# Kernel optimization log

Hardware: AMD Instinct MI355X
Metric: run time of the kernel (lower is better)

Reference implementation:

```python
import jax, jax.numpy as jnp
import numpy as np
from jax import lax

B, N, C = 8, 4096, 96
STRIDE, NSAMPLE, RADIUS = 4, 16, 0.1
C2 = 2 * C            # out_channels = 192 (also transfer in/out channels)
NPOINT = N // STRIDE  # 1024
EPS = 1e-5


def _fps(p, npoint):
    """Furthest point sampling. p: [B,N,3] -> idx [B,npoint] (starts at index 0)."""
    b, n, _ = p.shape
    def body(carry, _):
        mind, last = carry                       # [b,n], [b]
        lp = p[jnp.arange(b), last]              # [b,3]
        d = jnp.sum((p - lp[:, None, :]) ** 2, -1)
        mind = jnp.minimum(mind, d)
        nxt = jnp.argmax(mind, axis=1).astype(jnp.int32)
        return (mind, nxt), last
    init = (jnp.full((b, n), 1e10, p.dtype), jnp.zeros((b,), jnp.int32))
    (_, _), idxs = lax.scan(body, init, None, length=npoint)
    return jnp.transpose(idxs)                   # [b, npoint]


def _ball_query(new_p, p, radius, nsample):
    """First-nsample-in-index-order neighbors within radius; pad with first found."""
    n = p.shape[1]
    d2 = jnp.sum((new_p[:, :, None, :] - p[:, None, :, :]) ** 2, -1)  # [B,NP,N]
    order = jnp.where(d2 < radius * radius, jnp.arange(n, dtype=jnp.int32), n)
    vals, _ = lax.top_k(-order, nsample)         # k smallest 'order' values
    srt = -vals                                  # ascending valid indices, n = invalid
    return jnp.where(srt < n, srt, srt[..., :1]).astype(jnp.int32)


def _bn(y, g, b, m, v):
    """Eval-mode BatchNorm over channel axis 1."""
    shape = (1, -1) + (1,) * (y.ndim - 2)
    return (y - m.reshape(shape)) * (g.reshape(shape) / jnp.sqrt(v.reshape(shape) + EPS)) + b.reshape(shape)


def setup_inputs() -> dict:
    key = jax.random.key(0)
    ks = jax.random.split(key, 12)
    s = 1.0 / np.sqrt(C2)
    return {
        "p": jax.random.uniform(ks[0], (B, N, 3), jnp.float32),
        "x": jax.random.normal(ks[1], (B, C, N), jnp.float32),
        "Wt": jax.random.normal(ks[2], (C2, C2), jnp.float32) * s,
        "gt": 1.0 + 0.1 * jax.random.normal(ks[3], (C2,), jnp.float32),
        "bt": 0.1 * jax.random.normal(ks[4], (C2,), jnp.float32),
        "mt": 0.1 * jax.random.normal(ks[5], (C2,), jnp.float32),
        "vt": jax.random.uniform(ks[6], (C2,), jnp.float32, 0.5, 1.5),
        "Wc": jax.random.normal(ks[7], (C2, C2), jnp.float32) * s,
        "gc": 1.0 + 0.1 * jax.random.normal(ks[8], (C2,), jnp.float32),
        "bc": 0.1 * jax.random.normal(ks[9], (C2,), jnp.float32),
        "mc": 0.1 * jax.random.normal(ks[10], (C2,), jnp.float32),
        "vc": jax.random.uniform(ks[11], (C2,), jnp.float32, 0.5, 1.5),
    }


def reference(p, x, Wt, gt, bt, mt, vt, Wc, gc, bc, mc, vc):
    b = p.shape[0]
    bidx = jnp.arange(b)[:, None]
    # --- FPS sample + gather centers ---
    samp = _fps(p, NPOINT)                       # [B,NP]
    new_p = p[bidx, samp]                        # [B,NP,3]
    # --- ball-query grouping ---
    nbr = _ball_query(new_p, p, RADIUS, NSAMPLE)  # [B,NP,NS]
    bidx2 = jnp.arange(b)[:, None, None]
    gp = p[bidx2, nbr]                           # [B,NP,NS,3]
    dp = jnp.transpose(gp - new_p[:, :, None, :], (0, 3, 1, 2))  # [B,3,NP,NS]
    xt = jnp.transpose(x, (0, 2, 1))             # [B,N,C]
    gx = jnp.transpose(xt[bidx2, nbr], (0, 3, 1, 2))             # [B,C,NP,NS]
    cx = jnp.transpose(xt[bidx, samp], (0, 2, 1))[..., None]     # [B,C,NP,1]
    xj = jnp.concatenate([jnp.broadcast_to(cx, gx.shape), gx], axis=1)  # [B,2C,NP,NS]
    # --- act + transfer (1x1 conv + BN + relu) ---
    xj = jax.nn.relu(xj)
    xj = jax.nn.relu(_bn(jnp.einsum('oc,bcgs->bogs', Wt, xj), gt, bt, mt, vt))
    # --- PosPool sin/cos positional encoding ---
    fd = C2 // 6
    dim_mat = jnp.float32(500.0) ** (jnp.arange(fd, dtype=jnp.float32) / fd)
    pos = (50.0 * dp)[..., None] / dim_mat       # [B,3,NP,NS,fd]
    emb = jnp.concatenate([jnp.sin(pos), jnp.cos(pos)], -1)      # [B,3,NP,NS,2fd]
    emb = jnp.transpose(emb, (0, 1, 4, 2, 3)).reshape(xj.shape)  # [B,C2,NP,NS]
    agg = xj * emb + emb
    # --- max + mean pool over neighbors ---
    pooled = jnp.max(agg, -1) + jnp.mean(agg, -1)                # [B,C2,NP]
    # --- act + convs (1x1 conv + BN + relu) ---
    out = jax.nn.relu(_bn(jnp.einsum('oc,bcg->bog', Wc, jax.nn.relu(pooled)), gc, bc, mc, vc))
    return new_p, out
```

## Files before the change

### kernel.cpp

```cpp
#include <hip/hip_runtime.h>
#include <math.h>

#define BB 8
#define NN 4096
#define CC 96
#define C2 192
#define NP 1024
#define NS 16
#define FPT 8

#define SAMP_OFF   0u
#define NBR_OFF    32768u
#define WSW_OFF    655360u
#define B1_OFF     802816u
#define WCT_OFF    803584u
#define B2_OFF     951040u
#define ZT_OFF     958464u

template<int CTRL, int RM>
__device__ __forceinline__ unsigned long long dpp_mov64(unsigned long long k) {
    int tlo = __builtin_amdgcn_update_dpp(0, (int)(unsigned)(k & 0xffffffffull),
                                          CTRL, RM, 0xf, false);
    int thi = __builtin_amdgcn_update_dpp(0, (int)(unsigned)(k >> 32),
                                          CTRL, RM, 0xf, false);
    return ((unsigned long long)(unsigned)thi << 32) | (unsigned)tlo;
}

__global__ __launch_bounds__(512) void fps_prep_kernel(
        const float* __restrict__ p,
        const float* __restrict__ Wt, const float* __restrict__ gt,
        const float* __restrict__ bt, const float* __restrict__ mt,
        const float* __restrict__ vt, const float* __restrict__ Wc,
        const float* __restrict__ gc, const float* __restrict__ bc,
        const float* __restrict__ mc, const float* __restrict__ vc,
        float* __restrict__ Ws, float* __restrict__ beta1,
        float* __restrict__ WcT, float* __restrict__ beta2,
        int* __restrict__ samp, float* __restrict__ out) {
    if (blockIdx.x >= BB) {
        int i = (blockIdx.x - BB) * 512 + threadIdx.x;
        if (i < C2) {
            float s1 = gt[i] / sqrtf(vt[i] + 1e-5f);
            beta1[i] = bt[i] - mt[i] * s1;
            float s2 = gc[i] / sqrtf(vc[i] + 1e-5f);
            beta2[i] = bc[i] - mc[i] * s2;
        }
        if (i < 384 * 96) {
            int r = i / 96, c = i - r * 96;
            int o = (r < C2) ? r : r - C2;
            float s1 = gt[o] / sqrtf(vt[o] + 1e-5f);
            float w = (r < C2) ? Wt[o * C2 + c] : Wt[o * C2 + 96 + c];
            Ws[i] = w * s1;
        }
        if (i < C2 * C2) {
            int o = i / C2, c = i - o * C2;
            float s2 = gc[o] / sqrtf(vc[o] + 1e-5f);
            WcT[c * C2 + o] = Wc[i] * s2;
        }
        return;
    }
    int b = blockIdx.x;
    const float* pb = p + (size_t)b * NN * 3;
    __shared__ unsigned long long redk[2][8];
    __shared__ float4 redc[2][8];
    int tid = threadIdx.x;
    int jbase = tid * FPT;

    float c24[24];
    const float4* pb4 = (const float4*)(pb + (size_t)jbase * 3);
    #pragma unroll
    for (int i = 0; i < 6; ++i) ((float4*)c24)[i] = pb4[i];
    float px[FPT], py[FPT], pz[FPT], mind[FPT];
    #pragma unroll
    for (int i = 0; i < FPT; ++i) {
        px[i] = c24[3*i+0]; py[i] = c24[3*i+1]; pz[i] = c24[3*i+2];
        mind[i] = 1e10f;
    }

    int last = 0;
    float lx = pb[0], ly = pb[1], lz = pb[2];
    unsigned inv_base = 4095u - (unsigned)jbase;

    for (int it = 0; it < NP; ++it) {
        if (tid == 0) {
            samp[b * NP + it] = last;
            size_t o3 = ((size_t)b * NP + it) * 3;
            out[o3 + 0] = lx; out[o3 + 1] = ly; out[o3 + 2] = lz;
        }
        float m[FPT];
        #pragma unroll
        for (int i = 0; i < FPT; ++i) {
            float dx = __fsub_rn(px[i], lx);
            float dy = __fsub_rn(py[i], ly);
            float dz = __fsub_rn(pz[i], lz);
            float d = __fadd_rn(__fadd_rn(__fmul_rn(dx, dx), __fmul_rn(dy, dy)),
                                __fmul_rn(dz, dz));
            float mi = fminf(mind[i], d);
            mind[i] = mi;
            m[i] = mi;
        }
        float v4[4]; int i4v[4];
        #pragma unroll
        for (int q = 0; q < 4; ++q) {
            bool t = m[2*q+1] > m[2*q];
            v4[q] = t ? m[2*q+1] : m[2*q];
            i4v[q] = t ? 2*q+1 : 2*q;
        }
        float v2a[2]; int i2v[2];
        #pragma unroll
        for (int q = 0; q < 2; ++q) {
            bool t = v4[2*q+1] > v4[2*q];
            v2a[q] = t ? v4[2*q+1] : v4[2*q];
            i2v[q] = t ? i4v[2*q+1] : i4v[2*q];
        }
        bool tf = v2a[1] > v2a[0];
        float bv = tf ? v2a[1] : v2a[0];
        int ii  = tf ? i2v[1] : i2v[0];
        unsigned long long key =
            ((unsigned long long)__float_as_uint(bv) << 32)
            | (unsigned long long)(inv_base - (unsigned)ii);

        unsigned long long red = key, t;
        t = dpp_mov64<0x111, 0xf>(red); red = (t > red) ? t : red;
        t = dpp_mov64<0x112, 0xf>(red); red = (t > red) ? t : red;
        t = dpp_mov64<0x114, 0xf>(red); red = (t > red) ? t : red;
        t = dpp_mov64<0x118, 0xf>(red); red = (t > red) ? t : red;
        t = dpp_mov64<0x142, 0xa>(red); red = (t > red) ? t : red;
        t = dpp_mov64<0x143, 0xc>(red); red = (t > red) ? t : red;

        unsigned rlo = (unsigned)__builtin_amdgcn_readlane((int)(unsigned)(red & 0xffffffffull), 63);
        unsigned rhi = (unsigned)__builtin_amdgcn_readlane((int)(unsigned)(red >> 32), 63);
        unsigned long long wkey = ((unsigned long long)rhi << 32) | rlo;
        int buf = it & 1;
        if (key == wkey) {
            int wv = tid >> 6;
            redk[buf][wv] = wkey;
            redc[buf][wv] = make_float4(px[ii], py[ii], pz[ii], 0.0f);
        }
        __syncthreads();

        unsigned long long k0 = redk[buf][0], k1 = redk[buf][1];
        unsigned long long k2 = redk[buf][2], k3 = redk[buf][3];
        unsigned long long k4 = redk[buf][4], k5 = redk[buf][5];
        unsigned long long k6 = redk[buf][6], k7 = redk[buf][7];
        float4 c0 = redc[buf][0], c1 = redc[buf][1];
        float4 c2 = redc[buf][2], c3 = redc[buf][3];
        float4 c4 = redc[buf][4], c5 = redc[buf][5];
        float4 c6 = redc[buf][6], c7 = redc[buf][7];
        #define MRG(ka, ca, kb, cb) { bool tm = (kb) > (ka); \
            ka = tm ? (kb) : (ka); \
            ca.x = tm ? cb.x : ca.x; ca.y = tm ? cb.y : ca.y; ca.z = tm ? cb.z : ca.z; }
        MRG(k0, c0, k1, c1); MRG(k2, c2, k3, c3);
        MRG(k4, c4, k5, c5); MRG(k6, c6, k7, c7);
        MRG(k0, c0, k2, c2); MRG(k4, c4, k6, c6);
        MRG(k0, c0, k4, c4);
        #undef MRG
        last = 4095 - (int)(unsigned)(k0 & 0xffffffffull);
        lx = c0.x; ly = c0.y; lz = c0.z;
    }
}

__global__ __launch_bounds__(256) void bq_gemm_kernel(
        const float* __restrict__ p, const float* __restrict__ newp,
        int* __restrict__ nbr,
        const float* __restrict__ x, const float* __restrict__ Ws,
        float* __restrict__ zt) {
    __shared__ float smem[12352];
    int tid = threadIdx.x;

    if (blockIdx.x < 2048) {
        float* sx = smem;
        float* sy = smem + NN;
        float* sz = smem + 2 * NN;
        int blk = blockIdx.x;
        int b = blk >> 8;
        const float* pb = p + (size_t)b * NN * 3;
        for (int idx = tid; idx < NN; idx += 256) {
            sx[idx] = pb[idx * 3 + 0];
            sy[idx] = pb[idx * 3 + 1];
            sz[idx] = pb[idx * 3 + 2];
        }
        __syncthreads();
        int wave = tid >> 6, lane = tid & 63;
        int g = (blk & 255) * 4 + wave;
        int gidx = b * NP + g;
        float cx = newp[(size_t)gidx * 3 + 0];
        float cy = newp[(size_t)gidx * 3 + 1];
        float cz = newp[(size_t)gidx * 3 + 2];
        const float R2 = 0.01f;
        int cnt = 0, first = -1;
        for (int chunk = 0; chunk < NN / 64 && cnt < NS; ++chunk) {
            int j = chunk * 64 + lane;
            float dx = __fsub_rn(cx, sx[j]);
            float dy = __fsub_rn(cy, sy[j]);
            float dz = __fsub_rn(cz, sz[j]);
            float d2 = __fadd_rn(__fadd_rn(__fmul_rn(dx, dx), __fmul_rn(dy, dy)),
                                 __fmul_rn(dz, dz));
            unsigned long long mask = __ballot(d2 < R2);
            while (mask && cnt < NS) {
                int bit = __ffsll(mask) - 1;
                mask &= mask - 1;
                int idx = chunk * 64 + bit;
                if (first < 0) first = idx;
                if (lane == 0) nbr[(size_t)gidx * NS + cnt] = idx;
                ++cnt;
            }
        }
        if (lane == 0) {
            for (int i = cnt; i < NS; ++i) nbr[(size_t)gidx * NS + i] = first;
        }
    } else {
        float* xt = smem;
        float* wt = smem + 6144;
        int g = blockIdx.x - 2048;
        int b = g & 7;
        int t2 = g >> 3;
        int ob = t2 >> 6;
        int jt = t2 & 63;

        for (int idx = tid; idx < 96 * 64; idx += 256) {
            int c = idx >> 6, j = idx & 63;
            xt[c * 64 + j] = fmaxf(x[((size_t)b * CC + c) * NN + jt * 64 + j], 0.0f);
        }
        for (int idx = tid; idx < 64 * 96; idx += 256) {
            int r = idx / 96, c = idx - r * 96;
            wt[r * 97 + c] = Ws[(ob * 64 + r) * 96 + c];
        }
        __syncthreads();

        int ty = tid >> 4, tx = tid & 15;
        float acc[4][4] = {};
        for (int k = 0; k < 96; ++k) {
            float a0 = wt[(ty * 4 + 0) * 97 + k];
            float a1 = wt[(ty * 4 + 1) * 97 + k];
            float a2 = wt[(ty * 4 + 2) * 97 + k];
            float a3 = wt[(ty * 4 + 3) * 97 + k];
            float4 bv = *(const float4*)&xt[k * 64 + tx * 4];
            acc[0][0] = fmaf(a0, bv.x, acc[0][0]); acc[0][1] = fmaf(a0, bv.y, acc[0][1]);
            acc[0][2] = fmaf(a0, bv.z, acc[0][2]); acc[0][3] = fmaf(a0, bv.w, acc[0][3]);
            acc[1][0] = fmaf(a1, bv.x, acc[1][0]); acc[1][1] = fmaf(a1, bv.y, acc[1][1]);
            acc[1][2] = fmaf(a1, bv.z, acc[1][2]); acc[1][3] = fmaf(a1, bv.w, acc[1][3]);
            acc[2][0] = fmaf(a2, bv.x, acc[2][0]); acc[2][1] = fmaf(a2, bv.y, acc[2][1]);
            acc[2][2] = fmaf(a2, bv.z, acc[2][2]); acc[2][3] = fmaf(a2, bv.w, acc[2][3]);
            acc[3][0] = fmaf(a3, bv.x, acc[3][0]); acc[3][1] = fmaf(a3, bv.y, acc[3][1]);
            acc[3][2] = fmaf(a3, bv.z, acc[3][2]); acc[3][3] = fmaf(a3, bv.w, acc[3][3]);
        }
        for (int jj = 0; jj < 4; ++jj) {
            int j = jt * 64 + tx * 4 + jj;
            float4 v = make_float4(acc[0][jj], acc[1][jj], acc[2][jj], acc[3][jj]);
            *(float4*)&zt[((size_t)b * NN + j) * 384 + ob * 64 + ty * 4] = v;
        }
    }
}

__global__ __launch_bounds__(192) void fused_kernel(const float* __restrict__ p,
                                                    const float* __restrict__ newp,
                                                    const int* __restrict__ samp,
                                                    const int* __restrict__ nbr,
                                                    const float* __restrict__ zt,
                                                    const float* __restrict__ beta1,
                                                    const float* __restrict__ WcT,
                                                    const float* __restrict__ beta2,
                                                    float* __restrict__ out) {
    int blk = blockIdx.x;
    int b = blk >> 10, g = blk & 1023;
    int tid = threadIdx.x;
    __shared__ float dp[3][NS];
    __shared__ int nb[NS];
    __shared__ float pl[C2];

    if (tid < NS) {
        int j = nbr[(size_t)blk * NS + tid];
        nb[tid] = j;
        dp[0][tid] = p[((size_t)b * NN + j) * 3 + 0] - newp[(size_t)blk * 3 + 0];
        dp[1][tid] = p[((size_t)b * NN + j) * 3 + 1] - newp[(size_t)blk * 3 + 1];
        dp[2][tid] = p[((size_t)b * NN + j) * 3 + 2] - newp[(size_t)blk * 3 + 2];
    }
    __syncthreads();

    int o = tid;
    int sidx = samp[blk];
    float zc = zt[((size_t)b * NN + sidx) * 384 + o];
    float bet = beta1[o];
    int axis = o >> 6;
    int k = o & 63;
    int kk = (k < 32) ? k : k - 32;
    float dim = powf(500.0f, (float)kk * (1.0f / 32.0f));

    float mx = -3.4e38f, sm = 0.0f;
    for (int s = 0; s < NS; ++s) {
        float zn = zt[((size_t)b * NN + nb[s]) * 384 + C2 + o];
        float t = fmaxf(zc + zn + bet, 0.0f);
        float pos = (50.0f * dp[axis][s]) / dim;
        float e = (k < 32) ? sinf(pos) : cosf(pos);
        float a = fmaf(t, e, e);
        mx = fmaxf(mx, a);
        sm += a;
    }
    pl[o] = fmaxf(mx + sm * (1.0f / 16.0f), 0.0f);
    __syncthreads();

    float acc = 0.0f;
    for (int c = 0; c < C2; ++c) acc = fmaf(WcT[c * C2 + o], pl[c], acc);
    float res = fmaxf(acc + beta2[o], 0.0f);
    out[BB * NP * 3 + ((size_t)b * C2 + o) * NP + g] = res;
}

extern "C" void kernel_launch(void* const* d_in, const int* in_sizes, int n_in,
                              void* d_out, int out_size, void* d_ws, size_t ws_size,
                              hipStream_t stream) {
    (void)in_sizes; (void)n_in; (void)out_size; (void)ws_size;
    const float* p  = (const float*)d_in[0];
    const float* x  = (const float*)d_in[1];
    const float* Wt = (const float*)d_in[2];
    const float* gt = (const float*)d_in[3];
    const float* bt = (const float*)d_in[4];
    const float* mt = (const float*)d_in[5];
    const float* vt = (const float*)d_in[6];
    const float* Wc = (const float*)d_in[7];
    const float* gc = (const float*)d_in[8];
    const float* bc = (const float*)d_in[9];
    const float* mc = (const float*)d_in[10];
    const float* vc = (const float*)d_in[11];
    float* out = (float*)d_out;
    char* ws = (char*)d_ws;

    int*   samp  = (int*)(ws + SAMP_OFF);
    int*   nbr   = (int*)(ws + NBR_OFF);
    float* Ws    = (float*)(ws + WSW_OFF);
    float* beta1 = (float*)(ws + B1_OFF);
    float* WcT   = (float*)(ws + WCT_OFF);
    float* beta2 = (float*)(ws + B2_OFF);
    float* zt    = (float*)(ws + ZT_OFF);
    const float* newp = out;

    fps_prep_kernel<<<dim3(BB + 72), dim3(512), 0, stream>>>(
        p, Wt, gt, bt, mt, vt, Wc, gc, bc, mc, vc,
        Ws, beta1, WcT, beta2, samp, out);
    bq_gemm_kernel<<<dim3(2048 + 3072), dim3(256), 0, stream>>>(
        p, newp, nbr, x, Ws, zt);
    fused_kernel<<<dim3(BB * NP), dim3(192), 0, stream>>>(
        p, newp, samp, nbr, zt, beta1, WcT, beta2, out);
}
```

Baseline: 1.198 ms.

## Overlap GEMM with FPS in one launch and shrink FPS reduction to 4 waves

The transfer GEMM now runs in the same launch as furthest point sampling, so its blocks can fill the GPU while the 8 serial FPS blocks run. BN scaling of Wt is folded into the GEMM tile load, which removes the intermediate Ws buffer. FPS drops to 256 threads with 16 points each and replaces the 64-bit key DPP reduction with a float max reduction plus a ballot, which shortens the per-iteration critical path. Ball query becomes its own kernel after FPS. The risks are that GEMM blocks may contend with the FPS blocks for CU resources, and that per-thread register pressure in FPS rises.

```diff
diff --git a/kernel.cpp b/kernel.cpp
--- a/kernel.cpp
+++ b/kernel.cpp
@@ -7,7 +7,7 @@
 #define C2 192
 #define NP 1024
 #define NS 16
-#define FPT 8
+#define PPT 16
 
 #define SAMP_OFF   0u
 #define NBR_OFF    32768u
@@ -17,213 +17,52 @@
 #define B2_OFF     951040u
 #define ZT_OFF     958464u
 
+#define GEMM_OFF   152
+
 template<int CTRL, int RM>
-__device__ __forceinline__ unsigned long long dpp_mov64(unsigned long long k) {
-    int tlo = __builtin_amdgcn_update_dpp(0, (int)(unsigned)(k & 0xffffffffull),
-                                          CTRL, RM, 0xf, false);
-    int thi = __builtin_amdgcn_update_dpp(0, (int)(unsigned)(k >> 32),
-                                          CTRL, RM, 0xf, false);
-    return ((unsigned long long)(unsigned)thi << 32) | (unsigned)tlo;
-}
-
-__global__ __launch_bounds__(512) void fps_prep_kernel(
-        const float* __restrict__ p,
+__device__ __forceinline__ float dpp_maxf(float v) {
+    int t = __builtin_amdgcn_update_dpp(0, __float_as_int(v), CTRL, RM, 0xf, false);
+    return fmaxf(v, __int_as_float(t));
+}
+
+__global__ __launch_bounds__(256) void fps_prep_gemm_kernel(
+        const float* __restrict__ p, const float* __restrict__ x,
         const float* __restrict__ Wt, const float* __restrict__ gt,
         const float* __restrict__ bt, const float* __restrict__ mt,
         const float* __restrict__ vt, const float* __restrict__ Wc,
         const float* __restrict__ gc, const float* __restrict__ bc,
         const float* __restrict__ mc, const float* __restrict__ vc,
-        float* __restrict__ Ws, float* __restrict__ beta1,
-        float* __restrict__ WcT, float* __restrict__ beta2,
+        float* __restrict__ beta1, float* __restrict__ WcT,
+        float* __restrict__ beta2, float* __restrict__ zt,
         int* __restrict__ samp, float* __restrict__ out) {
-    if (blockIdx.x >= BB) {
-        int i = (blockIdx.x - BB) * 512 + threadIdx.x;
-        if (i < C2) {
-            float s1 = gt[i] / sqrtf(vt[i] + 1e-5f);
-            beta1[i] = bt[i] - mt[i] * s1;
-            float s2 = gc[i] / sqrtf(vc[i] + 1e-5f);
-            beta2[i] = bc[i] - mc[i] * s2;
-        }
-        if (i < 384 * 96) {
-            int r = i / 96, c = i - r * 96;
-            int o = (r < C2) ? r : r - C2;
-            float s1 = gt[o] / sqrtf(vt[o] + 1e-5f);
-            float w = (r < C2) ? Wt[o * C2 + c] : Wt[o * C2 + 96 + c];
-            Ws[i] = w * s1;
-        }
-        if (i < C2 * C2) {
-            int o = i / C2, c = i - o * C2;
-            float s2 = gc[o] / sqrtf(vc[o] + 1e-5f);
-            WcT[c * C2 + o] = Wc[i] * s2;
-        }
-        return;
-    }
-    int b = blockIdx.x;
-    const float* pb = p + (size_t)b * NN * 3;
-    __shared__ unsigned long long redk[2][8];
-    __shared__ float4 redc[2][8];
     int tid = threadIdx.x;
-    int jbase = tid * FPT;
-
-    float c24[24];
-    const float4* pb4 = (const float4*)(pb + (size_t)jbase * 3);
-    #pragma unroll
-    for (int i = 0; i < 6; ++i) ((float4*)c24)[i] = pb4[i];
-    float px[FPT], py[FPT], pz[FPT], mind[FPT];
-    #pragma unroll
-    for (int i = 0; i < FPT; ++i) {
-        px[i] = c24[3*i+0]; py[i] = c24[3*i+1]; pz[i] = c24[3*i+2];
-        mind[i] = 1e10f;
-    }
-
-    int last = 0;
-    float lx = pb[0], ly = pb[1], lz = pb[2];
-    unsigned inv_base = 4095u - (unsigned)jbase;
-
-    for (int it = 0; it < NP; ++it) {
-        if (tid == 0) {
-            samp[b * NP + it] = last;
-            size_t o3 = ((size_t)b * NP + it) * 3;
-            out[o3 + 0] = lx; out[o3 + 1] = ly; out[o3 + 2] = lz;
-        }
-        float m[FPT];
-        #pragma unroll
-        for (int i = 0; i < FPT; ++i) {
-            float dx = __fsub_rn(px[i], lx);
-            float dy = __fsub_rn(py[i], ly);
-            float dz = __fsub_rn(pz[i], lz);
-            float d = __fadd_rn(__fadd_rn(__fmul_rn(dx, dx), __fmul_rn(dy, dy)),
-                                __fmul_rn(dz, dz));
-            float mi = fminf(mind[i], d);
-            mind[i] = mi;
-            m[i] = mi;
-        }
-        float v4[4]; int i4v[4];
-        #pragma unroll
-        for (int q = 0; q < 4; ++q) {
-            bool t = m[2*q+1] > m[2*q];
-            v4[q] = t ? m[2*q+1] : m[2*q];
-            i4v[q] = t ? 2*q+1 : 2*q;
-        }
-        float v2a[2]; int i2v[2];
-        #pragma unroll
-        for (int q = 0; q < 2; ++q) {
-            bool t = v4[2*q+1] > v4[2*q];
-            v2a[q] = t ? v4[2*q+1] : v4[2*q];
-            i2v[q] = t ? i4v[2*q+1] : i4v[2*q];
-        }
-        bool tf = v2a[1] > v2a[0];
-        float bv = tf ? v2a[1] : v2a[0];
-        int ii  = tf ? i2v[1] : i2v[0];
-        unsigned long long key =
-            ((unsigned long long)__float_as_uint(bv) << 32)
-            | (unsigned long long)(inv_base - (unsigned)ii);
-
-        unsigned long long red = key, t;
-        t = dpp_mov64<0x111, 0xf>(red); red = (t > red) ? t : red;
-        t = dpp_mov64<0x112, 0xf>(red); red = (t > red) ? t : red;
-        t = dpp_mov64<0x114, 0xf>(red); red = (t > red) ? t : red;
-        t = dpp_mov64<0x118, 0xf>(red); red = (t > red) ? t : red;
-        t = dpp_mov64<0x142, 0xa>(red); red = (t > red) ? t : red;
-        t = dpp_mov64<0x143, 0xc>(red); red = (t > red) ? t : red;
-
-        unsigned rlo = (unsigned)__builtin_amdgcn_readlane((int)(unsigned)(red & 0xffffffffull), 63);
-        unsigned rhi = (unsigned)__builtin_amdgcn_readlane((int)(unsigned)(red >> 32), 63);
-        unsigned long long wkey = ((unsigned long long)rhi << 32) | rlo;
-        int buf = it & 1;
-        if (key == wkey) {
-            int wv = tid >> 6;
-            redk[buf][wv] = wkey;
-            redc[buf][wv] = make_float4(px[ii], py[ii], pz[ii], 0.0f);
-        }
-        __syncthreads();
-
-        unsigned long long k0 = redk[buf][0], k1 = redk[buf][1];
-        unsigned long long k2 = redk[buf][2], k3 = redk[buf][3];
-        unsigned long long k4 = redk[buf][4], k5 = redk[buf][5];
-        unsigned long long k6 = redk[buf][6], k7 = redk[buf][7];
-        float4 c0 = redc[buf][0], c1 = redc[buf][1];
-        float4 c2 = redc[buf][2], c3 = redc[buf][3];
-        float4 c4 = redc[buf][4], c5 = redc[buf][5];
-        float4 c6 = redc[buf][6], c7 = redc[buf][7];
-        #define MRG(ka, ca, kb, cb) { bool tm = (kb) > (ka); \
-            ka = tm ? (kb) : (ka); \
-            ca.x = tm ? cb.x : ca.x; ca.y = tm ? cb.y : ca.y; ca.z = tm ? cb.z : ca.z; }
-        MRG(k0, c0, k1, c1); MRG(k2, c2, k3, c3);
-        MRG(k4, c4, k5, c5); MRG(k6, c6, k7, c7);
-        MRG(k0, c0, k2, c2); MRG(k4, c4, k6, c6);
-        MRG(k0, c0, k4, c4);
-        #undef MRG
-        last = 4095 - (int)(unsigned)(k0 & 0xffffffffull);
-        lx = c0.x; ly = c0.y; lz = c0.z;
-    }
-}
-
-__global__ __launch_bounds__(256) void bq_gemm_kernel(
-        const float* __restrict__ p, const float* __restrict__ newp,
-        int* __restrict__ nbr,
-        const float* __restrict__ x, const float* __restrict__ Ws,
-        float* __restrict__ zt) {
-    __shared__ float smem[12352];
-    int tid = threadIdx.x;
-
-    if (blockIdx.x < 2048) {
-        float* sx = smem;
-        float* sy = smem + NN;
-        float* sz = smem + 2 * NN;
-        int blk = blockIdx.x;
-        int b = blk >> 8;
-        const float* pb = p + (size_t)b * NN * 3;
-        for (int idx = tid; idx < NN; idx += 256) {
-            sx[idx] = pb[idx * 3 + 0];
-            sy[idx] = pb[idx * 3 + 1];
-            sz[idx] = pb[idx * 3 + 2];
-        }
-        __syncthreads();
-        int wave = tid >> 6, lane = tid & 63;
-        int g = (blk & 255) * 4 + wave;
-        int gidx = b * NP + g;
-        float cx = newp[(size_t)gidx * 3 + 0];
-        float cy = newp[(size_t)gidx * 3 + 1];
-        float cz = newp[(size_t)gidx * 3 + 2];
-        const float R2 = 0.01f;
-        int cnt = 0, first = -1;
-        for (int chunk = 0; chunk < NN / 64 && cnt < NS; ++chunk) {
-            int j = chunk * 64 + lane;
-            float dx = __fsub_rn(cx, sx[j]);
-            float dy = __fsub_rn(cy, sy[j]);
-            float dz = __fsub_rn(cz, sz[j]);
-            float d2 = __fadd_rn(__fadd_rn(__fmul_rn(dx, dx), __fmul_rn(dy, dy)),
-                                 __fmul_rn(dz, dz));
-            unsigned long long mask = __ballot(d2 < R2);
-            while (mask && cnt < NS) {
-                int bit = __ffsll(mask) - 1;
-                mask &= mask - 1;
-                int idx = chunk * 64 + bit;
-                if (first < 0) first = idx;
-                if (lane == 0) nbr[(size_t)gidx * NS + cnt] = idx;
-                ++cnt;
-            }
-        }
-        if (lane == 0) {
-            for (int i = cnt; i < NS; ++i) nbr[(size_t)gidx * NS + i] = first;
-        }
-    } else {
+
+    if (blockIdx.x >= GEMM_OFF) {
+        __shared__ float smem[12416];
         float* xt = smem;
         float* wt = smem + 6144;
-        int g = blockIdx.x - 2048;
+        float* s1s = smem + 12352;
+        int g = blockIdx.x - GEMM_OFF;
         int b = g & 7;
         int t2 = g >> 3;
         int ob = t2 >> 6;
         int jt = t2 & 63;
 
+        if (tid < 64) {
+            int grow = ob * 64 + tid;
+            int o = (grow < C2) ? grow : grow - C2;
+            s1s[tid] = gt[o] / sqrtf(vt[o] + 1e-5f);
+        }
         for (int idx = tid; idx < 96 * 64; idx += 256) {
             int c = idx >> 6, j = idx & 63;
             xt[c * 64 + j] = fmaxf(x[((size_t)b * CC + c) * NN + jt * 64 + j], 0.0f);
         }
+        __syncthreads();
         for (int idx = tid; idx < 64 * 96; idx += 256) {
             int r = idx / 96, c = idx - r * 96;
-            wt[r * 97 + c] = Ws[(ob * 64 + r) * 96 + c];
+            int grow = ob * 64 + r;
+            float w = (grow < C2) ? Wt[grow * C2 + c] : Wt[(grow - C2) * C2 + 96 + c];
+            wt[r * 97 + c] = w * s1s[r];
         }
         __syncthreads();
 
@@ -249,6 +88,165 @@
             float4 v = make_float4(acc[0][jj], acc[1][jj], acc[2][jj], acc[3][jj]);
             *(float4*)&zt[((size_t)b * NN + j) * 384 + ob * 64 + ty * 4] = v;
         }
+        return;
+    }
+
+    if (blockIdx.x >= BB) {
+        int i = (blockIdx.x - BB) * 256 + tid;
+        if (i < C2) {
+            float s1 = gt[i] / sqrtf(vt[i] + 1e-5f);
+            beta1[i] = bt[i] - mt[i] * s1;
+            float s2 = gc[i] / sqrtf(vc[i] + 1e-5f);
+            beta2[i] = bc[i] - mc[i] * s2;
+        }
+        if (i < C2 * C2) {
+            int o = i / C2, c = i - o * C2;
+            float s2 = gc[o] / sqrtf(vc[o] + 1e-5f);
+            WcT[c * C2 + o] = Wc[i] * s2;
+        }
+        return;
+    }
+
+    {
+    int b = blockIdx.x;
+    const float* pb = p + (size_t)b * NN * 3;
+    __shared__ unsigned long long redk[2][4];
+    __shared__ float4 redc[2][4];
+    int jbase = tid * PPT;
+
+    float c48[48];
+    const float4* pb4 = (const float4*)(pb + (size_t)jbase * 3);
+    #pragma unroll
+    for (int i = 0; i < 12; ++i) ((float4*)c48)[i] = pb4[i];
+    float px[PPT], py[PPT], pz[PPT], mind[PPT];
+    #pragma unroll
+    for (int i = 0; i < PPT; ++i) {
+        px[i] = c48[3*i+0]; py[i] = c48[3*i+1]; pz[i] = c48[3*i+2];
+        mind[i] = 1e10f;
+    }
+
+    int last = 0;
+    float lx = pb[0], ly = pb[1], lz = pb[2];
+
+    for (int it = 0; it < NP; ++it) {
+        if (tid == 0) {
+            samp[b * NP + it] = last;
+            size_t o3 = ((size_t)b * NP + it) * 3;
+            out[o3 + 0] = lx; out[o3 + 1] = ly; out[o3 + 2] = lz;
+        }
+        float m[PPT];
+        #pragma unroll
+        for (int i = 0; i < PPT; ++i) {
+            float dx = __fsub_rn(px[i], lx);
+            float dy = __fsub_rn(py[i], ly);
+            float dz = __fsub_rn(pz[i], lz);
+            float d = __fadd_rn(__fadd_rn(__fmul_rn(dx, dx), __fmul_rn(dy, dy)),
+                                __fmul_rn(dz, dz));
+            float mi = fminf(mind[i], d);
+            mind[i] = mi;
+            m[i] = mi;
+        }
+        float v8[8]; int i8v[8];
+        #pragma unroll
+        for (int q = 0; q < 8; ++q) {
+            bool t = m[2*q+1] > m[2*q];
+            v8[q] = t ? m[2*q+1] : m[2*q];
+            i8v[q] = t ? 2*q+1 : 2*q;
+        }
+        float v4[4]; int i4v[4];
+        #pragma unroll
+        for (int q = 0; q < 4; ++q) {
+            bool t = v8[2*q+1] > v8[2*q];
+            v4[q] = t ? v8[2*q+1] : v8[2*q];
+            i4v[q] = t ? i8v[2*q+1] : i8v[2*q];
+        }
+        float v2a[2]; int i2v[2];
+        #pragma unroll
+        for (int q = 0; q < 2; ++q) {
+            bool t = v4[2*q+1] > v4[2*q];
+            v2a[q] = t ? v4[2*q+1] : v4[2*q];
+            i2v[q] = t ? i4v[2*q+1] : i4v[2*q];
+        }
+        bool tf = v2a[1] > v2a[0];
+        float bv = tf ? v2a[1] : v2a[0];
+        int ii  = tf ? i2v[1] : i2v[0];
+
+        float r = bv;
+        r = dpp_maxf<0x111, 0xf>(r);
+        r = dpp_maxf<0x112, 0xf>(r);
+        r = dpp_maxf<0x114, 0xf>(r);
+        r = dpp_maxf<0x118, 0xf>(r);
+        r = dpp_maxf<0x142, 0xa>(r);
+        r = dpp_maxf<0x143, 0xc>(r);
+        float wmax = __int_as_float(__builtin_amdgcn_readlane(__float_as_int(r), 63));
+
+        unsigned long long ball = __ballot(bv == wmax);
+        int winlane = (int)(__ffsll((long long)ball) - 1);
+        int buf = it & 1;
+        if ((tid & 63) == winlane) {
+            int wv = tid >> 6;
+            redk[buf][wv] = ((unsigned long long)__float_as_uint(bv) << 32)
+                            | (unsigned long long)(unsigned)(4095 - (jbase + ii));
+            redc[buf][wv] = make_float4(px[ii], py[ii], pz[ii], 0.0f);
+        }
+        __syncthreads();
+
+        unsigned long long k0 = redk[buf][0], k1 = redk[buf][1];
+        unsigned long long k2 = redk[buf][2], k3 = redk[buf][3];
+        float4 c0 = redc[buf][0], c1 = redc[buf][1];
+        float4 c2 = redc[buf][2], c3 = redc[buf][3];
+        #define MRG(ka, ca, kb, cb) { bool tm = (kb) > (ka); \
+            ka = tm ? (kb) : (ka); \
+            ca.x = tm ? cb.x : ca.x; ca.y = tm ? cb.y : ca.y; ca.z = tm ? cb.z : ca.z; }
+        MRG(k0, c0, k1, c1); MRG(k2, c2, k3, c3); MRG(k0, c0, k2, c2);
+        #undef MRG
+        last = 4095 - (int)(unsigned)(k0 & 0xffffffffull);
+        lx = c0.x; ly = c0.y; lz = c0.z;
+    }
+    }
+}
+
+__global__ __launch_bounds__(256) void ballquery_kernel(
+        const float* __restrict__ p, const float* __restrict__ newp,
+        int* __restrict__ nbr) {
+    __shared__ float sx[NN], sy[NN], sz[NN];
+    int blk = blockIdx.x;
+    int b = blk >> 8;
+    int tid = threadIdx.x;
+    const float* pb = p + (size_t)b * NN * 3;
+    for (int idx = tid; idx < NN; idx += 256) {
+        sx[idx] = pb[idx * 3 + 0];
+        sy[idx] = pb[idx * 3 + 1];
+        sz[idx] = pb[idx * 3 + 2];
+    }
+    __syncthreads();
+    int wave = tid >> 6, lane = tid & 63;
+    int g = (blk & 255) * 4 + wave;
+    int gidx = b * NP + g;
+    float cx = newp[(size_t)gidx * 3 + 0];
+    float cy = newp[(size_t)gidx * 3 + 1];
+    float cz = newp[(size_t)gidx * 3 + 2];
+    const float R2 = 0.01f;
+    int cnt = 0, first = -1;
+    for (int chunk = 0; chunk < NN / 64 && cnt < NS; ++chunk) {
+        int j = chunk * 64 + lane;
+        float dx = __fsub_rn(cx, sx[j]);
+        float dy = __fsub_rn(cy, sy[j]);
+        float dz = __fsub_rn(cz, sz[j]);
+        float d2 = __fadd_rn(__fadd_rn(__fmul_rn(dx, dx), __fmul_rn(dy, dy)),
+                             __fmul_rn(dz, dz));
+        unsigned long long mask = __ballot(d2 < R2);
+        while (mask && cnt < NS) {
+            int bit = __ffsll(mask) - 1;
+            mask &= mask - 1;
+            int idx = chunk * 64 + bit;
+            if (first < 0) first = idx;
+            if (lane == 0) nbr[(size_t)gidx * NS + cnt] = idx;
+            ++cnt;
+        }
+    }
+    if (lane == 0) {
+        for (int i = cnt; i < NS; ++i) nbr[(size_t)gidx * NS + i] = first;
     }
 }
 
@@ -326,18 +324,16 @@
 
     int*   samp  = (int*)(ws + SAMP_OFF);
     int*   nbr   = (int*)(ws + NBR_OFF);
-    float* Ws    = (float*)(ws + WSW_OFF);
     float* beta1 = (float*)(ws + B1_OFF);
     float* WcT   = (float*)(ws + WCT_OFF);
     float* beta2 = (float*)(ws + B2_OFF);
     float* zt    = (float*)(ws + ZT_OFF);
     const float* newp = out;
 
-    fps_prep_kernel<<<dim3(BB + 72), dim3(512), 0, stream>>>(
-        p, Wt, gt, bt, mt, vt, Wc, gc, bc, mc, vc,
-        Ws, beta1, WcT, beta2, samp, out);
-    bq_gemm_kernel<<<dim3(2048 + 3072), dim3(256), 0, stream>>>(
-        p, newp, nbr, x, Ws, zt);
+    fps_prep_gemm_kernel<<<dim3(GEMM_OFF + 3072), dim3(256), 0, stream>>>(
+        p, x, Wt, gt, bt, mt, vt, Wc, gc, bc, mc, vc,
+        beta1, WcT, beta2, zt, samp, out);
+    ballquery_kernel<<<dim3(2048), dim3(256), 0, stream>>>(p, newp, nbr);
     fused_kernel<<<dim3(BB * NP), dim3(192), 0, stream>>>(
         p, newp, samp, nbr, zt, beta1, WcT, beta2, out);
 }
```

New measurement: 1.501 ms. 25.3% more time.
